# Kernel optimization log

Measured on AMD Instinct MI355X. Metric: run time of the kernel, lower is better.

Reference implementation:

```python
import jax, jax.numpy as jnp
import numpy as np
import math

D_MODEL = 1024
N_HEADS = 16
D_HEAD = D_MODEL // N_HEADS
NUM_BUCKETS = 32
MAX_DISTANCE = 128


def _relative_position_bucket(relative_position):
    # bidirectional T5-style bucketing
    num_buckets = NUM_BUCKETS // 2
    buckets = (relative_position > 0).astype(jnp.int32) * num_buckets
    rp = jnp.abs(relative_position)
    max_exact = num_buckets // 2
    is_small = rp < max_exact
    rpf = jnp.maximum(rp, 1).astype(jnp.float32)  # avoid log(0); masked by is_small
    rp_large = max_exact + (
        jnp.log(rpf / max_exact) / math.log(MAX_DISTANCE / max_exact) * (num_buckets - max_exact)
    ).astype(jnp.int32)
    rp_large = jnp.minimum(rp_large, num_buckets - 1)
    return buckets + jnp.where(is_small, rp, rp_large)


def _compute_bias(q_len, k_len, rel_emb):
    context_pos = jnp.arange(q_len, dtype=jnp.int32)[:, None]
    memory_pos = jnp.arange(k_len, dtype=jnp.int32)[None, :]
    rp_bucket = _relative_position_bucket(memory_pos - context_pos)  # [Tq, Tk]
    values = rel_emb[rp_bucket]                 # [Tq, Tk, H]
    return jnp.transpose(values, (2, 0, 1))[None]  # [1, H, Tq, Tk]


def setup_inputs() -> dict:
    key = jax.random.key(0)
    ks = jax.random.split(key, 8)
    B, T = 4, 2048
    return {
        "query": jax.random.normal(ks[0], (B, T, D_MODEL), dtype=jnp.float32),
        "key": jax.random.normal(ks[1], (B, T, D_MODEL), dtype=jnp.float32),
        "value": jax.random.normal(ks[2], (B, T, D_MODEL), dtype=jnp.float32),
        "Wq": jax.random.normal(ks[3], (D_MODEL, D_MODEL), dtype=jnp.float32) * 0.02,
        "Wk": jax.random.normal(ks[4], (D_MODEL, D_MODEL), dtype=jnp.float32) * 0.02,
        "Wv": jax.random.normal(ks[5], (D_MODEL, D_MODEL), dtype=jnp.float32) * 0.02,
        "Wo": jax.random.normal(ks[6], (D_MODEL, D_MODEL), dtype=jnp.float32) * 0.02,
        "rel_emb": jax.random.normal(ks[7], (NUM_BUCKETS, N_HEADS), dtype=jnp.float32) * 0.02,
    }


def reference(query, key, value, Wq, Wk, Wv, Wo, rel_emb):
    B, Tq, _ = query.shape
    Tk = key.shape[1]
    # torch nn.Linear(bias=False): y = x @ W.T
    q = (query @ Wq.T).reshape(B, Tq, N_HEADS, D_HEAD).transpose(0, 2, 1, 3)  # [B,H,Tq,Dh]
    k = (key @ Wk.T).reshape(B, Tk, N_HEADS, D_HEAD).transpose(0, 2, 1, 3)
    v = (value @ Wv.T).reshape(B, Tk, N_HEADS, D_HEAD).transpose(0, 2, 1, 3)
    scores = jnp.einsum("bhqd,bhkd->bhqk", q, k) / math.sqrt(D_HEAD)  # [B,H,Tq,Tk]
    position_bias = _compute_bias(Tq, Tk, rel_emb)
    scores = scores + position_bias
    attn = jax.nn.softmax(scores, axis=-1)
    out = jnp.einsum("bhqk,bhkd->bhqd", attn, v)
    out = out.transpose(0, 2, 1, 3).reshape(B, Tq, D_MODEL)
    out = out @ Wo.T
    return out, position_bias
```

## Files before the change

kernel.cpp:

```cpp
#include <hip/hip_runtime.h>

typedef _Float16 half8 __attribute__((ext_vector_type(8)));
typedef _Float16 half4 __attribute__((ext_vector_type(4)));
typedef float f32x4 __attribute__((ext_vector_type(4)));

#define DEV __device__ __forceinline__

DEV f32x4 mfma16(half8 a, half8 b, f32x4 c) {
  return __builtin_amdgcn_mfma_f32_16x16x32_f16(a, b, c, 0, 0, 0);
}

DEV void load_lds16(const void* g, void* l) {
  __builtin_amdgcn_global_load_lds((const __attribute__((address_space(1))) void*)g,
                                   (__attribute__((address_space(3))) void*)l, 16, 0, 0);
}

DEV int t5_bucket(int delta) {
  int b = (delta > 0) ? 16 : 0;
  int rp = delta < 0 ? -delta : delta;
  if (rp < 8) return b + rp;
  float lg = logf((float)rp * 0.125f);
  int large = 8 + (int)(lg / 2.772588722239781f * 8.0f);
  if (large > 15) large = 15;
  return b + large;
}

DEV float bias_val(const float* rel, int n, int h) {
  return rel[t5_bucket(n - 2047) * 16 + h];
}

__global__ __launch_bounds__(256) void prep_kernel(
    const float* __restrict__ q, const float* __restrict__ k, const float* __restrict__ v,
    const float* __restrict__ wq, const float* __restrict__ wk, const float* __restrict__ wv,
    const float* __restrict__ wo, const float* __restrict__ rel,
    _Float16* __restrict__ Xh, _Float16* __restrict__ W3h, _Float16* __restrict__ Woh,
    _Float16* __restrict__ BiasH, float* __restrict__ Bf) {
  unsigned u = blockIdx.x * 256u + threadIdx.x;
  if (u < 6291456u) {
    unsigned p = u / 2097152u, r = u - p * 2097152u;
    const float4* s = (const float4*)(p == 0 ? q : p == 1 ? k : v);
    float4 x = s[r];
    half4 hv = {(_Float16)x.x, (_Float16)x.y, (_Float16)x.z, (_Float16)x.w};
    *(half4*)(Xh + (size_t)p * 8388608u + (size_t)r * 4u) = hv;
  } else if (u < 7340032u) {
    unsigned t = u - 6291456u;
    const float4* s;
    _Float16* d;
    if (t < 786432u) {
      unsigned p = t / 262144u, r = t - p * 262144u;
      s = (const float4*)(p == 0 ? wq : p == 1 ? wk : wv) + r;
      d = W3h + (size_t)p * 1048576u + (size_t)r * 4u;
    } else {
      unsigned r = t - 786432u;
      s = (const float4*)wo + r;
      d = Woh + (size_t)r * 4u;
    }
    float4 x = *s;
    half4 hv = {(_Float16)x.x, (_Float16)x.y, (_Float16)x.z, (_Float16)x.w};
    *(half4*)d = hv;
  } else {
    unsigned t = u - 7340032u;
    int h = (int)(t >> 12), n = (int)(t & 4095u);
    Bf[h * 4096 + n] = (n <= 4094) ? bias_val(rel, n, h) : 0.f;
    half4 hv;
#pragma unroll
    for (int j = 0; j < 4; j++) {
      float bv = (n + j <= 4094) ? bias_val(rel, n + j, h) * 1.4426950408889634f : 0.f;
      hv[j] = (_Float16)bv;
    }
    *(half4*)(BiasH + (size_t)(h * 4096 + n) * 4u) = hv;
  }
}

template <int MODE>
__global__ __launch_bounds__(256) void gemm128(
    const _Float16* __restrict__ A, const _Float16* __restrict__ B,
    _Float16* __restrict__ D0, _Float16* __restrict__ D1, _Float16* __restrict__ D2,
    float* __restrict__ F) {
  __shared__ _Float16 Asm[128 * 64];
  __shared__ _Float16 Bsm[128 * 64];
  const int tid = threadIdx.x;
  const int w = tid >> 6, L = tid & 63;
  const int g = L >> 4, c15 = L & 15;
  const int m0 = blockIdx.x * 128, n0 = blockIdx.y * 128;
  const int z = blockIdx.z;
  const _Float16* Ab = A + ((size_t)z * 8192 + m0) * 1024;
  const _Float16* Bb = B + ((size_t)z * 1024 + n0) * 1024;
  f32x4 acc[4][4] = {};
  const int mw = (w & 1) * 64, nw = (w >> 1) * 64;
  const int wbase = tid & ~63;
  for (int k0 = 0; k0 < 1024; k0 += 64) {
    __syncthreads();
#pragma unroll
    for (int c = 0; c < 4; c++) {
      int i = c * 256 + tid;
      int row = i >> 3, pc = i & 7;
      int lc = pc ^ ((row >> 1) & 7);
      load_lds16(Ab + (size_t)row * 1024 + k0 + lc * 8, Asm + (c * 256 + wbase) * 8);
      load_lds16(Bb + (size_t)row * 1024 + k0 + lc * 8, Bsm + (c * 256 + wbase) * 8);
    }
    __builtin_amdgcn_s_waitcnt(0);
    __syncthreads();
#pragma unroll
    for (int kc = 0; kc < 2; kc++) {
      half8 af[4], bf[4];
#pragma unroll
      for (int t = 0; t < 4; t++) {
        int rowA = mw + t * 16 + c15;
        int pcA = (kc * 4 + g) ^ ((rowA >> 1) & 7);
        af[t] = *(const half8*)(Asm + rowA * 64 + pcA * 8);
        int rowB = nw + t * 16 + c15;
        int pcB = (kc * 4 + g) ^ ((rowB >> 1) & 7);
        bf[t] = *(const half8*)(Bsm + rowB * 64 + pcB * 8);
      }
#pragma unroll
      for (int mt = 0; mt < 4; mt++)
#pragma unroll
        for (int nt = 0; nt < 4; nt++)
          acc[mt][nt] = mfma16(bf[nt], af[mt], acc[mt][nt]);
    }
  }
  if (MODE == 0) {
    float scale = (z == 0) ? 0.18033688011112042f : 1.0f;
    _Float16* dst = (z == 0) ? D0 : (z == 1) ? D1 : D2;
#pragma unroll
    for (int mt = 0; mt < 4; mt++) {
      int m = m0 + mw + mt * 16 + c15;
      int bb = m >> 11, t = m & 2047;
#pragma unroll
      for (int nt = 0; nt < 4; nt++) {
        int n = n0 + nw + nt * 16 + g * 4;
        half4 hv;
#pragma unroll
        for (int r = 0; r < 4; r++) hv[r] = (_Float16)(acc[mt][nt][r] * scale);
        *(half4*)(dst + (((size_t)bb * 16 + (n >> 6)) * 2048 + t) * 64 + (n & 63)) = hv;
      }
    }
  } else {
#pragma unroll
    for (int mt = 0; mt < 4; mt++) {
      int m = m0 + mw + mt * 16 + c15;
#pragma unroll
      for (int nt = 0; nt < 4; nt++) {
        int n = n0 + nw + nt * 16 + g * 4;
        float4 fv = make_float4(acc[mt][nt][0], acc[mt][nt][1], acc[mt][nt][2], acc[mt][nt][3]);
        *(float4*)(F + (size_t)m * 1024 + n) = fv;
      }
    }
  }
}

__global__ __launch_bounds__(256) void transpose_v(const _Float16* __restrict__ V,
                                                   _Float16* __restrict__ Vt) {
  int bh = blockIdx.z * 16 + blockIdx.y;
  const _Float16* Vb = V + (size_t)bh * 2048 * 64;
  _Float16* Vtb = Vt + (size_t)bh * 80 * 2048;
  int tid = threadIdx.x;
  if (blockIdx.x == 32) {
    _Float16 one = (_Float16)1.0f, zero = (_Float16)0.0f;
#pragma unroll
    for (int j = 0; j < 16; j++) {
      half8 vv;
#pragma unroll
      for (int e = 0; e < 8; e++) vv[e] = (j == 0) ? one : zero;
      *(half8*)(Vtb + (size_t)(64 + j) * 2048 + tid * 8) = vv;
    }
    return;
  }
  __shared__ _Float16 tileS[64][64];
  int t0 = blockIdx.x * 64;
#pragma unroll
  for (int c = 0; c < 2; c++) {
    int i = c * 256 + tid;
    int row = i >> 3, col = (i & 7) * 8;
    half8 vv = *(const half8*)(Vb + (size_t)(t0 + row) * 64 + col);
    int xr = 8 * ((col >> 3) & 7);
#pragma unroll
    for (int j = 0; j < 8; j++) tileS[col + j][row ^ xr] = vv[j];
  }
  __syncthreads();
  int d = tid >> 2, c = (tid & 3) * 16;
  int xr = 8 * ((d >> 3) & 7);
  half8 o0 = *(const half8*)(&tileS[d][c ^ xr]);
  half8 o1 = *(const half8*)(&tileS[d][(c + 8) ^ xr]);
  *(half8*)(Vtb + (size_t)d * 2048 + t0 + c) = o0;
  *(half8*)(Vtb + (size_t)d * 2048 + t0 + c + 8) = o1;
}

__global__ __launch_bounds__(256, 2) void flash_attn(
    const _Float16* __restrict__ Q, const _Float16* __restrict__ K,
    const _Float16* __restrict__ Vt, const _Float16* __restrict__ BiasH,
    _Float16* __restrict__ AO) {
  __shared__ _Float16 Kst[2][64 * 64];
  __shared__ _Float16 Vst[2][80 * 64];
  __shared__ half4 biasS[2304];
  __shared__ _Float16 pS[4][64][40];
  const int b = blockIdx.z, h = blockIdx.x, qb = blockIdx.y * 256;
  const int bh = b * 16 + h;
  const _Float16* Qb = Q + (size_t)bh * 2048 * 64;
  const _Float16* Kb = K + (size_t)bh * 2048 * 64;
  const _Float16* Vtb = Vt + (size_t)bh * 80 * 2048;
  const int tid = threadIdx.x, w = tid >> 6, L = tid & 63;
  const int g = L >> 4, c15 = L & 15;
  const int wbase = tid & ~63;
  const int idx0 = 1792 - qb;

  auto stage = [&](int buf, int kk) {
#pragma unroll
    for (int c = 0; c < 2; c++) {
      int i = c * 256 + tid;
      int row = i >> 3, pc = i & 7, lc = pc ^ ((row >> 1) & 7);
      load_lds16(Kb + (size_t)(kk + row) * 64 + lc * 8, &Kst[buf][(c * 256 + wbase) * 8]);
    }
#pragma unroll
    for (int c = 0; c < 2; c++) {
      int i = c * 256 + tid;
      int row = i >> 3, pc = i & 7, lc = pc ^ ((row >> 1) & 7);
      load_lds16(Vtb + (size_t)row * 2048 + kk + lc * 8, &Vst[buf][(c * 256 + wbase) * 8]);
    }
    if (tid < 128) {
      int i = 512 + tid;
      int row = i >> 3, pc = i & 7, lc = pc ^ ((row >> 1) & 7);
      load_lds16(Vtb + (size_t)row * 2048 + kk + lc * 8, &Vst[buf][(512 + wbase) * 8]);
    }
  };

  stage(0, 0);
  for (int i = tid; i < 2304; i += 256)
    biasS[i] = *(const half4*)(BiasH + (size_t)(h * 4096 + idx0 + i) * 4u);
  half8 qf[4][2];
#pragma unroll
  for (int r2 = 0; r2 < 4; r2++)
#pragma unroll
    for (int kc = 0; kc < 2; kc++)
      qf[r2][kc] =
          *(const half8*)(Qb + (size_t)(qb + w * 64 + r2 * 16 + c15) * 64 + kc * 32 + g * 8);
  f32x4 O[4][5] = {};
  __builtin_amdgcn_s_waitcnt(0);
  __syncthreads();

  for (int kt = 0; kt < 32; kt++) {
    const int cur = kt & 1, nxt = cur ^ 1;
    if (kt < 31) stage(nxt, (kt + 1) * 64);
#pragma unroll
    for (int p = 0; p < 2; p++) {
      half8 kf[2][2];
#pragma unroll
      for (int nt2 = 0; nt2 < 2; nt2++)
#pragma unroll
        for (int kc = 0; kc < 2; kc++) {
          int row = (2 * p + nt2) * 16 + c15;
          int pc = (kc * 4 + g) ^ ((row >> 1) & 7);
          kf[nt2][kc] = *(const half8*)(&Kst[cur][row * 64 + pc * 8]);
        }
      half8 vf[5];
#pragma unroll
      for (int dt = 0; dt < 5; dt++) {
        int row = dt * 16 + c15;
        int pc = (p * 4 + g) ^ ((row >> 1) & 7);
        vf[dt] = *(const half8*)(&Vst[cur][row * 64 + pc * 8]);
      }
#pragma unroll
      for (int r2 = 0; r2 < 4; r2++) {
        int qloc = w * 64 + r2 * 16 + c15;
#pragma unroll
        for (int nt2 = 0; nt2 < 2; nt2++) {
          f32x4 z = {};
          f32x4 s0 = mfma16(kf[nt2][0], qf[r2][0], z);
          f32x4 S = mfma16(kf[nt2][1], qf[r2][1], s0);
          half4 bv = biasS[kt * 64 + p * 32 + nt2 * 16 + g * 4 + 255 - qloc];
          half4 pv;
#pragma unroll
          for (int r = 0; r < 4; r++)
            pv[r] = (_Float16)__builtin_amdgcn_exp2f(S[r] + (float)bv[r]);
          *(half4*)(&pS[w][r2 * 16 + c15][nt2 * 16 + g * 4]) = pv;
        }
      }
      __builtin_amdgcn_s_waitcnt(0xc07f);
      half8 pa[4];
#pragma unroll
      for (int r2 = 0; r2 < 4; r2++) pa[r2] = *(const half8*)(&pS[w][r2 * 16 + c15][g * 8]);
#pragma unroll
      for (int r2 = 0; r2 < 4; r2++)
#pragma unroll
        for (int dt = 0; dt < 5; dt++) O[r2][dt] = mfma16(vf[dt], pa[r2], O[r2][dt]);
    }
    __builtin_amdgcn_s_waitcnt(0);
    __syncthreads();
  }
#pragma unroll
  for (int r2 = 0; r2 < 4; r2++) {
    float linv = 1.0f / __shfl(O[r2][4][0], c15, 64);
    int qg = qb + w * 64 + r2 * 16 + c15;
    _Float16* dst = AO + ((size_t)(b * 2048 + qg)) * 1024 + h * 64;
#pragma unroll
    for (int dt = 0; dt < 4; dt++) {
      half4 ov;
#pragma unroll
      for (int r = 0; r < 4; r++) ov[r] = (_Float16)(O[r2][dt][r] * linv);
      *(half4*)(dst + dt * 16 + g * 4) = ov;
    }
  }
}

__global__ __launch_bounds__(256) void bias_out_k(const float* __restrict__ Bf,
                                                  float4* __restrict__ out2) {
  unsigned u = blockIdx.x * 256u + threadIdx.x;
  int hh = (int)(u >> 20);
  unsigned rem = u & 1048575u;
  int i = (int)(rem >> 9);
  int j4 = (int)(rem & 511u) * 4;
  const float* p = Bf + hh * 4096 + j4 - i + 2047;
  out2[u] = make_float4(p[0], p[1], p[2], p[3]);
}

extern "C" void kernel_launch(void* const* d_in, const int* in_sizes, int n_in,
                              void* d_out, int out_size, void* d_ws, size_t ws_size,
                              hipStream_t stream) {
  const float* q = (const float*)d_in[0];
  const float* k = (const float*)d_in[1];
  const float* v = (const float*)d_in[2];
  const float* wq = (const float*)d_in[3];
  const float* wk = (const float*)d_in[4];
  const float* wv = (const float*)d_in[5];
  const float* wo = (const float*)d_in[6];
  const float* rel = (const float*)d_in[7];

  _Float16* Xh = (_Float16*)d_ws;
  _Float16* W3h = Xh + 3u * 8388608u;
  _Float16* Woh = W3h + 3u * 1048576u;
  _Float16* Qh = Woh + 1048576u;
  _Float16* Kh = Qh + 8388608u;
  _Float16* Vh = Kh + 8388608u;
  _Float16* Vth = Vh + 8388608u;
  _Float16* AOh = Vth + 10485760u;
  _Float16* BiasH = AOh + 8388608u;
  float* Bf = (float*)(BiasH + 262144u);
  float* outp = (float*)d_out;

  prep_kernel<<<28928, 256, 0, stream>>>(q, k, v, wq, wk, wv, wo, rel, Xh, W3h, Woh, BiasH, Bf);
  gemm128<0><<<dim3(64, 8, 3), 256, 0, stream>>>(Xh, W3h, Qh, Kh, Vh, nullptr);
  transpose_v<<<dim3(33, 16, 4), 256, 0, stream>>>(Vh, Vth);
  flash_attn<<<dim3(16, 8, 4), 256, 0, stream>>>(Qh, Kh, Vth, BiasH, AOh);
  gemm128<1><<<dim3(64, 8, 1), 256, 0, stream>>>(AOh, Woh, nullptr, nullptr, nullptr, outp);
  bias_out_k<<<65536, 256, 0, stream>>>(Bf, (float4*)(outp + 8388608u));
}
```

Before: 591.1 us.

## Load K and V fragments directly from global memory instead of LDS staging

Drops the double-buffered LDS staging of K and transposed V tiles. Each wave now reads its MFMA fragments straight from global memory, relying on L2/L1 caching, and the per-tile block barrier is removed. It also raises wave priority around the PV MFMA block. This frees LDS and removes synchronisation, at the cost of redundant global loads across the four waves and exposed load latency with no explicit prefetch.

```diff
diff --git a/kernel.cpp b/kernel.cpp
--- a/kernel.cpp
+++ b/kernel.cpp
@@ -191,8 +191,6 @@
     const _Float16* __restrict__ Q, const _Float16* __restrict__ K,
     const _Float16* __restrict__ Vt, const _Float16* __restrict__ BiasH,
     _Float16* __restrict__ AO) {
-  __shared__ _Float16 Kst[2][64 * 64];
-  __shared__ _Float16 Vst[2][80 * 64];
   __shared__ half4 biasS[2304];
   __shared__ _Float16 pS[4][64][40];
   const int b = blockIdx.z, h = blockIdx.x, qb = blockIdx.y * 256;
@@ -202,30 +200,8 @@
   const _Float16* Vtb = Vt + (size_t)bh * 80 * 2048;
   const int tid = threadIdx.x, w = tid >> 6, L = tid & 63;
   const int g = L >> 4, c15 = L & 15;
-  const int wbase = tid & ~63;
   const int idx0 = 1792 - qb;
 
-  auto stage = [&](int buf, int kk) {
-#pragma unroll
-    for (int c = 0; c < 2; c++) {
-      int i = c * 256 + tid;
-      int row = i >> 3, pc = i & 7, lc = pc ^ ((row >> 1) & 7);
-      load_lds16(Kb + (size_t)(kk + row) * 64 + lc * 8, &Kst[buf][(c * 256 + wbase) * 8]);
-    }
-#pragma unroll
-    for (int c = 0; c < 2; c++) {
-      int i = c * 256 + tid;
-      int row = i >> 3, pc = i & 7, lc = pc ^ ((row >> 1) & 7);
-      load_lds16(Vtb + (size_t)row * 2048 + kk + lc * 8, &Vst[buf][(c * 256 + wbase) * 8]);
-    }
-    if (tid < 128) {
-      int i = 512 + tid;
-      int row = i >> 3, pc = i & 7, lc = pc ^ ((row >> 1) & 7);
-      load_lds16(Vtb + (size_t)row * 2048 + kk + lc * 8, &Vst[buf][(512 + wbase) * 8]);
-    }
-  };
-
-  stage(0, 0);
   for (int i = tid; i < 2304; i += 256)
     biasS[i] = *(const half4*)(BiasH + (size_t)(h * 4096 + idx0 + i) * 4u);
   half8 qf[4][2];
@@ -236,30 +212,23 @@
       qf[r2][kc] =
           *(const half8*)(Qb + (size_t)(qb + w * 64 + r2 * 16 + c15) * 64 + kc * 32 + g * 8);
   f32x4 O[4][5] = {};
-  __builtin_amdgcn_s_waitcnt(0);
   __syncthreads();
 
   for (int kt = 0; kt < 32; kt++) {
-    const int cur = kt & 1, nxt = cur ^ 1;
-    if (kt < 31) stage(nxt, (kt + 1) * 64);
 #pragma unroll
     for (int p = 0; p < 2; p++) {
+      const int kk = kt * 64 + p * 32;
       half8 kf[2][2];
 #pragma unroll
       for (int nt2 = 0; nt2 < 2; nt2++)
 #pragma unroll
-        for (int kc = 0; kc < 2; kc++) {
-          int row = (2 * p + nt2) * 16 + c15;
-          int pc = (kc * 4 + g) ^ ((row >> 1) & 7);
-          kf[nt2][kc] = *(const half8*)(&Kst[cur][row * 64 + pc * 8]);
-        }
+        for (int kc = 0; kc < 2; kc++)
+          kf[nt2][kc] =
+              *(const half8*)(Kb + (size_t)(kk + nt2 * 16 + c15) * 64 + kc * 32 + g * 8);
       half8 vf[5];
 #pragma unroll
-      for (int dt = 0; dt < 5; dt++) {
-        int row = dt * 16 + c15;
-        int pc = (p * 4 + g) ^ ((row >> 1) & 7);
-        vf[dt] = *(const half8*)(&Vst[cur][row * 64 + pc * 8]);
-      }
+      for (int dt = 0; dt < 5; dt++)
+        vf[dt] = *(const half8*)(Vtb + (size_t)(dt * 16 + c15) * 2048 + kk + g * 8);
 #pragma unroll
       for (int r2 = 0; r2 < 4; r2++) {
         int qloc = w * 64 + r2 * 16 + c15;
@@ -280,13 +249,13 @@
       half8 pa[4];
 #pragma unroll
       for (int r2 = 0; r2 < 4; r2++) pa[r2] = *(const half8*)(&pS[w][r2 * 16 + c15][g * 8]);
+      __builtin_amdgcn_s_setprio(1);
 #pragma unroll
       for (int r2 = 0; r2 < 4; r2++)
 #pragma unroll
         for (int dt = 0; dt < 5; dt++) O[r2][dt] = mfma16(vf[dt], pa[r2], O[r2][dt]);
-    }
-    __builtin_amdgcn_s_waitcnt(0);
-    __syncthreads();
+      __builtin_amdgcn_s_setprio(0);
+    }
   }
 #pragma unroll
   for (int r2 = 0; r2 < 4; r2++) {
```

Result: slower. 617.4 us (+4.5%).

## Fuse V transpose into projection GEMM epilogue and bias output into prep kernel

Applied to the files above, without the earlier changes.

The V projection GEMM now writes its output directly in transposed layout, which removes the separate transpose kernel and its intermediate V buffer. The position-bias output is computed directly inside the prep kernel from rel_emb instead of a separate kernel that reads a staged bias table. The ones/zeros padding rows of Vt are also filled in prep. In the flash-attention PV MFMA loop, s_setprio raises wave priority. The transposed epilogue writes scalar halfs with a 2048 stride, which is less coalesced than before, and the bias output now runs the log-based bucket computation per element.

```diff
diff --git a/kernel.cpp b/kernel.cpp
--- a/kernel.cpp
+++ b/kernel.cpp
@@ -34,7 +34,7 @@
     const float* __restrict__ wq, const float* __restrict__ wk, const float* __restrict__ wv,
     const float* __restrict__ wo, const float* __restrict__ rel,
     _Float16* __restrict__ Xh, _Float16* __restrict__ W3h, _Float16* __restrict__ Woh,
-    _Float16* __restrict__ BiasH, float* __restrict__ Bf) {
+    _Float16* __restrict__ BiasH, float4* __restrict__ out2, _Float16* __restrict__ Vth) {
   unsigned u = blockIdx.x * 256u + threadIdx.x;
   if (u < 6291456u) {
     unsigned p = u / 2097152u, r = u - p * 2097152u;
@@ -58,10 +58,9 @@
     float4 x = *s;
     half4 hv = {(_Float16)x.x, (_Float16)x.y, (_Float16)x.z, (_Float16)x.w};
     *(half4*)d = hv;
-  } else {
+  } else if (u < 7405568u) {
     unsigned t = u - 7340032u;
     int h = (int)(t >> 12), n = (int)(t & 4095u);
-    Bf[h * 4096 + n] = (n <= 4094) ? bias_val(rel, n, h) : 0.f;
     half4 hv;
 #pragma unroll
     for (int j = 0; j < 4; j++) {
@@ -69,13 +68,36 @@
       hv[j] = (_Float16)bv;
     }
     *(half4*)(BiasH + (size_t)(h * 4096 + n) * 4u) = hv;
+  } else if (u < 24182784u) {
+    unsigned vv = u - 7405568u;
+    int h = (int)(vv >> 20);
+    unsigned rem = vv & 1048575u;
+    int i = (int)(rem >> 9);
+    int j4 = (int)(rem & 511u) * 4;
+    int nb = j4 - i + 2047;
+    float f0 = bias_val(rel, nb, h);
+    float f1 = bias_val(rel, nb + 1, h);
+    float f2 = bias_val(rel, nb + 2, h);
+    float f3 = bias_val(rel, nb + 3, h);
+    out2[vv] = make_float4(f0, f1, f2, f3);
+  } else {
+    unsigned t5 = u - 24182784u;
+    int bh = (int)(t5 >> 12);
+    unsigned rr = t5 & 4095u;
+    int row16 = (int)(rr >> 8);
+    int col8 = (int)(rr & 255u) * 8;
+    _Float16 one = (_Float16)1.0f, zero = (_Float16)0.0f;
+    half8 ov;
+#pragma unroll
+    for (int e = 0; e < 8; e++) ov[e] = (row16 == 0) ? one : zero;
+    *(half8*)(Vth + (size_t)bh * 163840u + (size_t)(64 + row16) * 2048u + col8) = ov;
   }
 }
 
 template <int MODE>
 __global__ __launch_bounds__(256) void gemm128(
     const _Float16* __restrict__ A, const _Float16* __restrict__ B,
-    _Float16* __restrict__ D0, _Float16* __restrict__ D1, _Float16* __restrict__ D2,
+    _Float16* __restrict__ D0, _Float16* __restrict__ D1, _Float16* __restrict__ Vt,
     float* __restrict__ F) {
   __shared__ _Float16 Asm[128 * 64];
   __shared__ _Float16 Bsm[128 * 64];
@@ -121,19 +143,35 @@
     }
   }
   if (MODE == 0) {
-    float scale = (z == 0) ? 0.18033688011112042f : 1.0f;
-    _Float16* dst = (z == 0) ? D0 : (z == 1) ? D1 : D2;
-#pragma unroll
-    for (int mt = 0; mt < 4; mt++) {
-      int m = m0 + mw + mt * 16 + c15;
-      int bb = m >> 11, t = m & 2047;
-#pragma unroll
-      for (int nt = 0; nt < 4; nt++) {
-        int n = n0 + nw + nt * 16 + g * 4;
-        half4 hv;
-#pragma unroll
-        for (int r = 0; r < 4; r++) hv[r] = (_Float16)(acc[mt][nt][r] * scale);
-        *(half4*)(dst + (((size_t)bb * 16 + (n >> 6)) * 2048 + t) * 64 + (n & 63)) = hv;
+    if (z == 2) {
+#pragma unroll
+      for (int mt = 0; mt < 4; mt++) {
+        int m = m0 + mw + mt * 16 + c15;
+        int bb = m >> 11, t = m & 2047;
+#pragma unroll
+        for (int nt = 0; nt < 4; nt++) {
+          int n = n0 + nw + nt * 16 + g * 4;
+          _Float16* vt =
+              Vt + (((size_t)(bb * 16 + (n >> 6)) * 80 + (n & 63)) * 2048 + t);
+#pragma unroll
+          for (int r = 0; r < 4; r++) vt[(size_t)r * 2048] = (_Float16)acc[mt][nt][r];
+        }
+      }
+    } else {
+      float scale = (z == 0) ? 0.18033688011112042f : 1.0f;
+      _Float16* dst = (z == 0) ? D0 : D1;
+#pragma unroll
+      for (int mt = 0; mt < 4; mt++) {
+        int m = m0 + mw + mt * 16 + c15;
+        int bb = m >> 11, t = m & 2047;
+#pragma unroll
+        for (int nt = 0; nt < 4; nt++) {
+          int n = n0 + nw + nt * 16 + g * 4;
+          half4 hv;
+#pragma unroll
+          for (int r = 0; r < 4; r++) hv[r] = (_Float16)(acc[mt][nt][r] * scale);
+          *(half4*)(dst + (((size_t)bb * 16 + (n >> 6)) * 2048 + t) * 64 + (n & 63)) = hv;
+        }
       }
     }
   } else {
@@ -148,43 +186,6 @@
       }
     }
   }
-}
-
-__global__ __launch_bounds__(256) void transpose_v(const _Float16* __restrict__ V,
-                                                   _Float16* __restrict__ Vt) {
-  int bh = blockIdx.z * 16 + blockIdx.y;
-  const _Float16* Vb = V + (size_t)bh * 2048 * 64;
-  _Float16* Vtb = Vt + (size_t)bh * 80 * 2048;
-  int tid = threadIdx.x;
-  if (blockIdx.x == 32) {
-    _Float16 one = (_Float16)1.0f, zero = (_Float16)0.0f;
-#pragma unroll
-    for (int j = 0; j < 16; j++) {
-      half8 vv;
-#pragma unroll
-      for (int e = 0; e < 8; e++) vv[e] = (j == 0) ? one : zero;
-      *(half8*)(Vtb + (size_t)(64 + j) * 2048 + tid * 8) = vv;
-    }
-    return;
-  }
-  __shared__ _Float16 tileS[64][64];
-  int t0 = blockIdx.x * 64;
-#pragma unroll
-  for (int c = 0; c < 2; c++) {
-    int i = c * 256 + tid;
-    int row = i >> 3, col = (i & 7) * 8;
-    half8 vv = *(const half8*)(Vb + (size_t)(t0 + row) * 64 + col);
-    int xr = 8 * ((col >> 3) & 7);
-#pragma unroll
-    for (int j = 0; j < 8; j++) tileS[col + j][row ^ xr] = vv[j];
-  }
-  __syncthreads();
-  int d = tid >> 2, c = (tid & 3) * 16;
-  int xr = 8 * ((d >> 3) & 7);
-  half8 o0 = *(const half8*)(&tileS[d][c ^ xr]);
-  half8 o1 = *(const half8*)(&tileS[d][(c + 8) ^ xr]);
-  *(half8*)(Vtb + (size_t)d * 2048 + t0 + c) = o0;
-  *(half8*)(Vtb + (size_t)d * 2048 + t0 + c + 8) = o1;
 }
 
 __global__ __launch_bounds__(256, 2) void flash_attn(
@@ -280,10 +281,12 @@
       half8 pa[4];
 #pragma unroll
       for (int r2 = 0; r2 < 4; r2++) pa[r2] = *(const half8*)(&pS[w][r2 * 16 + c15][g * 8]);
+      __builtin_amdgcn_s_setprio(1);
 #pragma unroll
       for (int r2 = 0; r2 < 4; r2++)
 #pragma unroll
         for (int dt = 0; dt < 5; dt++) O[r2][dt] = mfma16(vf[dt], pa[r2], O[r2][dt]);
+      __builtin_amdgcn_s_setprio(0);
     }
     __builtin_amdgcn_s_waitcnt(0);
     __syncthreads();
@@ -301,17 +304,6 @@
       *(half4*)(dst + dt * 16 + g * 4) = ov;
     }
   }
-}
-
-__global__ __launch_bounds__(256) void bias_out_k(const float* __restrict__ Bf,
-                                                  float4* __restrict__ out2) {
-  unsigned u = blockIdx.x * 256u + threadIdx.x;
-  int hh = (int)(u >> 20);
-  unsigned rem = u & 1048575u;
-  int i = (int)(rem >> 9);
-  int j4 = (int)(rem & 511u) * 4;
-  const float* p = Bf + hh * 4096 + j4 - i + 2047;
-  out2[u] = make_float4(p[0], p[1], p[2], p[3]);
 }
 
 extern "C" void kernel_launch(void* const* d_in, const int* in_sizes, int n_in,
@@ -331,17 +323,15 @@
   _Float16* Woh = W3h + 3u * 1048576u;
   _Float16* Qh = Woh + 1048576u;
   _Float16* Kh = Qh + 8388608u;
-  _Float16* Vh = Kh + 8388608u;
-  _Float16* Vth = Vh + 8388608u;
+  _Float16* Vth = Kh + 8388608u;
   _Float16* AOh = Vth + 10485760u;
   _Float16* BiasH = AOh + 8388608u;
-  float* Bf = (float*)(BiasH + 262144u);
   float* outp = (float*)d_out;
-
-  prep_kernel<<<28928, 256, 0, stream>>>(q, k, v, wq, wk, wv, wo, rel, Xh, W3h, Woh, BiasH, Bf);
-  gemm128<0><<<dim3(64, 8, 3), 256, 0, stream>>>(Xh, W3h, Qh, Kh, Vh, nullptr);
-  transpose_v<<<dim3(33, 16, 4), 256, 0, stream>>>(Vh, Vth);
+  float4* out2 = (float4*)(outp + 8388608u);
+
+  prep_kernel<<<95488, 256, 0, stream>>>(q, k, v, wq, wk, wv, wo, rel, Xh, W3h, Woh, BiasH,
+                                         out2, Vth);
+  gemm128<0><<<dim3(64, 8, 3), 256, 0, stream>>>(Xh, W3h, Qh, Kh, Vth, nullptr);
   flash_attn<<<dim3(16, 8, 4), 256, 0, stream>>>(Qh, Kh, Vth, BiasH, AOh);
   gemm128<1><<<dim3(64, 8, 1), 256, 0, stream>>>(AOh, Woh, nullptr, nullptr, nullptr, outp);
-  bias_out_k<<<65536, 256, 0, stream>>>(Bf, (float4*)(outp + 8388608u));
-}
+}
```

After: 604.1 us. 2.2% more time.

## Fuse position-bias output writes into flash attention loop with nontemporal stores

Applied to the files above, without the earlier changes.

Removes the separate bias_out_k launch and has each flash_attn block write its share of the 256 MB fp32 position_bias output, interleaved with the attention K-loop, using nontemporal stores. The aim is to overlap this memory-bound write with the compute-bound attention. It also raises wave priority around the PV MFMAs and replaces the full waitcnt with a partial vmcnt wait so the bias stores stay in flight across the barrier. The added stores and extra registers could contend with the K/V staging loads and lower occupancy.

```diff
diff --git a/kernel.cpp b/kernel.cpp
--- a/kernel.cpp
+++ b/kernel.cpp
@@ -190,7 +190,8 @@
 __global__ __launch_bounds__(256, 2) void flash_attn(
     const _Float16* __restrict__ Q, const _Float16* __restrict__ K,
     const _Float16* __restrict__ Vt, const _Float16* __restrict__ BiasH,
-    _Float16* __restrict__ AO) {
+    _Float16* __restrict__ AO, const float* __restrict__ Bf,
+    f32x4* __restrict__ out2) {
   __shared__ _Float16 Kst[2][64 * 64];
   __shared__ _Float16 Vst[2][80 * 64];
   __shared__ half4 biasS[2304];
@@ -204,6 +205,8 @@
   const int g = L >> 4, c15 = L & 15;
   const int wbase = tid & ~63;
   const int idx0 = 1792 - qb;
+  const unsigned u0 =
+      ((unsigned)(blockIdx.z * 8 + blockIdx.y) * 16 + blockIdx.x) * 32768u + tid;
 
   auto stage = [&](int buf, int kk) {
 #pragma unroll
@@ -241,6 +244,20 @@
 
   for (int kt = 0; kt < 32; kt++) {
     const int cur = kt & 1, nxt = cur ^ 1;
+    float bo[4][4];
+    unsigned uu[4];
+#pragma unroll
+    for (int j = 0; j < 4; j++) {
+      unsigned u = u0 + (unsigned)(kt * 4 + j) * 256u;
+      uu[j] = u;
+      int hh = (int)(u >> 20);
+      unsigned rem = u & 1048575u;
+      int i = (int)(rem >> 9);
+      int j4 = (int)(rem & 511u) * 4;
+      const float* p = Bf + hh * 4096 + j4 - i + 2047;
+#pragma unroll
+      for (int e = 0; e < 4; e++) bo[j][e] = p[e];
+    }
     if (kt < 31) stage(nxt, (kt + 1) * 64);
 #pragma unroll
     for (int p = 0; p < 2; p++) {
@@ -280,13 +297,22 @@
       half8 pa[4];
 #pragma unroll
       for (int r2 = 0; r2 < 4; r2++) pa[r2] = *(const half8*)(&pS[w][r2 * 16 + c15][g * 8]);
+      __builtin_amdgcn_s_setprio(1);
 #pragma unroll
       for (int r2 = 0; r2 < 4; r2++)
 #pragma unroll
         for (int dt = 0; dt < 5; dt++) O[r2][dt] = mfma16(vf[dt], pa[r2], O[r2][dt]);
-    }
-    __builtin_amdgcn_s_waitcnt(0);
-    __syncthreads();
+      __builtin_amdgcn_s_setprio(0);
+    }
+#pragma unroll
+    for (int j = 0; j < 4; j++) {
+      f32x4 fv = {bo[j][0], bo[j][1], bo[j][2], bo[j][3]};
+      __builtin_nontemporal_store(fv, out2 + uu[j]);
+    }
+    asm volatile("s_waitcnt vmcnt(4) lgkmcnt(0)" ::: "memory");
+    __builtin_amdgcn_sched_barrier(0);
+    __builtin_amdgcn_s_barrier();
+    __builtin_amdgcn_sched_barrier(0);
   }
 #pragma unroll
   for (int r2 = 0; r2 < 4; r2++) {
@@ -301,17 +327,6 @@
       *(half4*)(dst + dt * 16 + g * 4) = ov;
     }
   }
-}
-
-__global__ __launch_bounds__(256) void bias_out_k(const float* __restrict__ Bf,
-                                                  float4* __restrict__ out2) {
-  unsigned u = blockIdx.x * 256u + threadIdx.x;
-  int hh = (int)(u >> 20);
-  unsigned rem = u & 1048575u;
-  int i = (int)(rem >> 9);
-  int j4 = (int)(rem & 511u) * 4;
-  const float* p = Bf + hh * 4096 + j4 - i + 2047;
-  out2[u] = make_float4(p[0], p[1], p[2], p[3]);
 }
 
 extern "C" void kernel_launch(void* const* d_in, const int* in_sizes, int n_in,
@@ -341,7 +356,7 @@
   prep_kernel<<<28928, 256, 0, stream>>>(q, k, v, wq, wk, wv, wo, rel, Xh, W3h, Woh, BiasH, Bf);
   gemm128<0><<<dim3(64, 8, 3), 256, 0, stream>>>(Xh, W3h, Qh, Kh, Vh, nullptr);
   transpose_v<<<dim3(33, 16, 4), 256, 0, stream>>>(Vh, Vth);
-  flash_attn<<<dim3(16, 8, 4), 256, 0, stream>>>(Qh, Kh, Vth, BiasH, AOh);
+  flash_attn<<<dim3(16, 8, 4), 256, 0, stream>>>(Qh, Kh, Vth, BiasH, AOh, Bf,
+                                                 (f32x4*)(outp + 8388608u));
   gemm128<1><<<dim3(64, 8, 1), 256, 0, stream>>>(AOh, Woh, nullptr, nullptr, nullptr, outp);
-  bias_out_k<<<65536, 256, 0, stream>>>(Bf, (float4*)(outp + 8388608u));
-}
+}
```

Measured after the change: 531.7 us. 10.0% less time.
